# Kernel optimization log

Hardware: AMD Instinct MI355X
Metric: run time of the kernel (lower is better)

Reference implementation:

```python
import jax, jax.numpy as jnp
import numpy as np

MARGIN = 0.3  # hard-coded in all three MarginRankingLoss instances


def setup_inputs() -> dict:
    key = jax.random.key(0)
    k1, k2, k3, k4 = jax.random.split(key, 4)
    n, d, num_ids = 4096, 2048, 100
    inputs = jax.random.normal(k1, (n, d), dtype=jnp.float32)
    targets_a = jax.random.randint(k2, (n,), 0, num_ids, dtype=jnp.int64)
    targets_b = jax.random.randint(k3, (n,), 0, num_ids, dtype=jnp.int64)
    lam = jax.random.uniform(k4, (), dtype=jnp.float32)
    epoch = 60
    return {"inputs": inputs, "targets_a": targets_a, "targets_b": targets_b,
            "lam": lam, "epoch": epoch}


def reference(inputs, targets_a, targets_b, lam, epoch):
    # pairwise euclidean distance: dist[i,j] = ||x_i - x_j||
    sq = jnp.sum(inputs * inputs, axis=1)                      # [n]
    dist = sq[:, None] + sq[None, :] - 2.0 * (inputs @ inputs.T)
    dist = jnp.sqrt(jnp.clip(dist, 1e-12))                     # [n, n]

    ma = targets_a[:, None] == targets_a[None, :]
    mb = targets_b[:, None] == targets_b[None, :]
    m_same_ab = ma & mb                                        # same a AND b (incl. diagonal)
    m_same_or = (ma & ~mb) | (~ma & mb)                        # exactly one of a/b matches
    m_dif_ab = ~ma & ~mb                                       # neither matches

    ninf = -jnp.inf
    pinf = jnp.inf
    hp = jnp.max(jnp.where(m_same_ab, dist, ninf), axis=1)     # hardest positive
    hn = jnp.min(jnp.where(m_dif_ab, dist, pinf), axis=1)      # hardest negative
    max_or = jnp.max(jnp.where(m_same_or, dist, ninf), axis=1)
    min_or = jnp.min(jnp.where(m_same_or, dist, pinf), axis=1)

    use_or = m_same_or.any(axis=1) & (epoch > 50)
    sp = jnp.where(use_or, max_or, hp)
    sn = jnp.where(use_or, min_or, hn)

    # MarginRankingLoss(x1, x2, y=1) = mean(relu(x2 - x1 + margin))
    loss_1 = jnp.mean(jnp.maximum(0.0, hp - hn + MARGIN))
    loss_2 = jnp.mean(jnp.maximum(0.0, sp - hn + MARGIN))
    loss_3 = jnp.mean(jnp.maximum(0.0, hp - sn + MARGIN))
    return loss_1 + loss_2 + loss_3
```

## Files before the change

### kernel.cpp

```cpp
#include <hip/hip_runtime.h>
#include <hip/hip_bf16.h>

#define NROW 4096
#define KDIM 2048
#define ROWB (KDIM * 2)
#define BT 128
#define NB (NROW / BT)
#define BK 32
#define NT (KDIM / BK)
#define KTBUF 16384
#define AB_OFF 8192
#define PHI(r) ((((r) >> 1) & 3) << 4)

typedef __attribute__((ext_vector_type(8))) short bf16x8;
typedef __attribute__((ext_vector_type(4))) float f32x4;
typedef __attribute__((ext_vector_type(4))) unsigned short u16x4;

#define MFMA16(a, b, c) __builtin_amdgcn_mfma_f32_16x16x32_bf16((a), (b), (c), 0, 0, 0)

__device__ __forceinline__ unsigned short f2bf(float x) {
    unsigned u = __float_as_uint(x);
    unsigned r = (u + 0x7FFFu + ((u >> 16) & 1u)) >> 16;
    return (unsigned short)r;
}
__device__ __forceinline__ float bf2f(unsigned short b) {
    return __uint_as_float(((unsigned)b) << 16);
}

__global__ __launch_bounds__(256) void k_convert(const float* __restrict__ X,
                                                 unsigned short* __restrict__ Xb,
                                                 float* __restrict__ sqv,
                                                 unsigned* __restrict__ hp,
                                                 unsigned* __restrict__ hn,
                                                 unsigned* __restrict__ mor,
                                                 unsigned* __restrict__ mir,
                                                 float* __restrict__ out) {
    const int row = blockIdx.x;
    const int t = threadIdx.x;
    if (row < 16) {
        const int i = row * 256 + t;
        hp[i] = 0u;
        hn[i] = 0x7F800000u;
        mor[i] = 0u;
        mir[i] = 0x7F800000u;
        if (i == 0) out[0] = 0.f;
    }
    const float4* xr = (const float4*)(X + (size_t)row * KDIM);
    unsigned short* br = Xb + (size_t)row * KDIM;
    float acc = 0.f;
#pragma unroll
    for (int it = 0; it < 2; ++it) {
        int idx = t * 2 + it;
        float4 v = xr[idx];
        u16x4 b;
        b.x = f2bf(v.x); b.y = f2bf(v.y); b.z = f2bf(v.z); b.w = f2bf(v.w);
        float f0 = bf2f(b.x), f1 = bf2f(b.y), f2 = bf2f(b.z), f3 = bf2f(b.w);
        acc += f0 * f0 + f1 * f1 + f2 * f2 + f3 * f3;
        *(u16x4*)(br + idx * 4) = b;
    }
#pragma unroll
    for (int s = 32; s > 0; s >>= 1) acc += __shfl_xor(acc, s);
    __shared__ float red[4];
    const int lane = t & 63, wid = t >> 6;
    if (lane == 0) red[wid] = acc;
    __syncthreads();
    if (t == 0) sqv[row] = red[0] + red[1] + red[2] + red[3];
}

__global__ __launch_bounds__(256, 3) void k_gemm(const unsigned short* __restrict__ Xb,
                                                 const float* __restrict__ sqv,
                                                 const int* __restrict__ ta,
                                                 const int* __restrict__ tb,
                                                 unsigned int* __restrict__ hp,
                                                 unsigned int* __restrict__ hn,
                                                 unsigned int* __restrict__ mor,
                                                 unsigned int* __restrict__ mir) {
    __shared__ char lds[4 * KTBUF];
    int rem = blockIdx.x;
    int bi = 0;
    while (rem >= NB - bi) { rem -= NB - bi; ++bi; }
    const int bj = bi + rem;

    const int t = threadIdx.x;
    const int lane = t & 63;
    const int w = t >> 6;
    const int wm = w >> 1;
    const int wn = w & 1;
    const int l15 = lane & 15;
    const int kg16 = (lane >> 4) * 16;
    const char* xbase = (const char*)Xb;

    const int swz = ((l15 >> 1) & 3) << 4;
    const int akbase = (wm * 64 + l15) * 64 + (kg16 ^ swz);
    const int bkbase = AB_OFF + (wn * 64 + l15) * 64 + (kg16 ^ swz);

    f32x4 acc[4][4] = {};

#define STAGE(tt)                                                             \
    do {                                                                      \
        _Pragma("unroll")                                                     \
        for (int isb_ = 0; isb_ < 2; ++isb_) {                                \
            _Pragma("unroll")                                                 \
            for (int q_ = 0; q_ < 2; ++q_) {                                  \
                const int row_ = q_ * 64 + (t >> 2);                          \
                const int gr_ = (isb_ ? bj : bi) * BT + row_;                 \
                const char* gsrc_ = xbase + (size_t)gr_ * ROWB +              \
                                    (size_t)(tt) * 64 +                       \
                                    (((t & 3) * 16) ^ PHI(row_));             \
                char* ldst_ = lds + ((tt) & 3) * KTBUF + isb_ * AB_OFF +      \
                              row_ * 64 + (t & 3) * 16;                       \
                __builtin_amdgcn_global_load_lds(                             \
                    (const __attribute__((address_space(1))) void*)gsrc_,     \
                    (__attribute__((address_space(3))) void*)ldst_, 16, 0, 0);\
            }                                                                 \
        }                                                                     \
    } while (0)

    STAGE(0);
    STAGE(1);
    STAGE(2);

    for (int tk = 0; tk < NT; ++tk) {
        if (tk < NT - 2)
            asm volatile("s_waitcnt vmcnt(8)" ::: "memory");
        else if (tk == NT - 2)
            asm volatile("s_waitcnt vmcnt(4)" ::: "memory");
        else
            asm volatile("s_waitcnt vmcnt(0)" ::: "memory");
        __builtin_amdgcn_s_barrier();

        const char* buf = lds + (tk & 3) * KTBUF;
        bf16x8 af[4], bfr[4];
#pragma unroll
        for (int m = 0; m < 4; ++m)
            af[m] = *(const bf16x8*)(buf + akbase + m * 1024);
#pragma unroll
        for (int n = 0; n < 4; ++n)
            bfr[n] = *(const bf16x8*)(buf + bkbase + n * 1024);

        if (tk + 3 < NT) STAGE(tk + 3);

#pragma unroll
        for (int m = 0; m < 4; ++m)
#pragma unroll
            for (int n = 0; n < 4; ++n)
                acc[m][n] = MFMA16(af[m], bfr[n], acc[m][n]);
    }
#undef STAGE

    float sqj[4];
    int taj[4], tbj[4];
#pragma unroll
    for (int n = 0; n < 4; ++n) {
        int j = bj * BT + wn * 64 + n * 16 + l15;
        sqj[n] = sqv[j];
        taj[n] = ta[j];
        tbj[n] = tb[j];
    }
    const float INF = __uint_as_float(0x7F800000u);

    float chp[4], chn[4], cmo[4], cmi[4];
#pragma unroll
    for (int n = 0; n < 4; ++n) {
        chp[n] = 0.f; chn[n] = INF; cmo[n] = 0.f; cmi[n] = INF;
    }

#pragma unroll
    for (int m = 0; m < 4; ++m) {
#pragma unroll
        for (int reg = 0; reg < 4; ++reg) {
            const int i = bi * BT + wm * 64 + m * 16 + (lane >> 4) * 4 + reg;
            const float sqi = sqv[i];
            const int tai = ta[i], tbi = tb[i];
            float vhp = 0.f, vhn = INF, vmo = 0.f, vmi = INF;
#pragma unroll
            for (int n = 0; n < 4; ++n) {
                float d2 = fmaxf(sqi + sqj[n] - 2.f * acc[m][n][reg], 1e-12f);
                bool ma = (tai == taj[n]), mb = (tbi == tbj[n]);
                if (ma && mb) {
                    vhp = fmaxf(vhp, d2);
                    chp[n] = fmaxf(chp[n], d2);
                } else if (ma != mb) {
                    vmo = fmaxf(vmo, d2);
                    vmi = fminf(vmi, d2);
                    cmo[n] = fmaxf(cmo[n], d2);
                    cmi[n] = fminf(cmi[n], d2);
                } else {
                    vhn = fminf(vhn, d2);
                    chn[n] = fminf(chn[n], d2);
                }
            }
#pragma unroll
            for (int s = 1; s < 16; s <<= 1) {
                vhp = fmaxf(vhp, __shfl_xor(vhp, s, 16));
                vhn = fminf(vhn, __shfl_xor(vhn, s, 16));
                vmo = fmaxf(vmo, __shfl_xor(vmo, s, 16));
                vmi = fminf(vmi, __shfl_xor(vmi, s, 16));
            }
            if (l15 == 0) {
                if (vhp > 0.f) atomicMax(&hp[i], __float_as_uint(vhp));
                if (vhn < INF) atomicMin(&hn[i], __float_as_uint(vhn));
                if (vmo > 0.f) {
                    atomicMax(&mor[i], __float_as_uint(vmo));
                    atomicMin(&mir[i], __float_as_uint(vmi));
                }
            }
        }
    }

    if (bi != bj) {
#pragma unroll
        for (int n = 0; n < 4; ++n) {
            float a = chp[n], b = chn[n], c = cmo[n], d = cmi[n];
            a = fmaxf(a, __shfl_xor(a, 16)); a = fmaxf(a, __shfl_xor(a, 32));
            b = fminf(b, __shfl_xor(b, 16)); b = fminf(b, __shfl_xor(b, 32));
            c = fmaxf(c, __shfl_xor(c, 16)); c = fmaxf(c, __shfl_xor(c, 32));
            d = fminf(d, __shfl_xor(d, 16)); d = fminf(d, __shfl_xor(d, 32));
            if (lane < 16) {
                const int j = bj * BT + wn * 64 + n * 16 + lane;
                if (a > 0.f) atomicMax(&hp[j], __float_as_uint(a));
                if (b < INF) atomicMin(&hn[j], __float_as_uint(b));
                if (c > 0.f) {
                    atomicMax(&mor[j], __float_as_uint(c));
                    atomicMin(&mir[j], __float_as_uint(d));
                }
            }
        }
    }
}

__global__ __launch_bounds__(256) void k_final(const unsigned* __restrict__ hp,
                                               const unsigned* __restrict__ hn,
                                               const unsigned* __restrict__ mor,
                                               const unsigned* __restrict__ mir,
                                               const int* __restrict__ epoch_p,
                                               float* __restrict__ out) {
    const int t = threadIdx.x;
    const int i = blockIdx.x * 256 + t;
    const bool eok = (*epoch_p > 50);
    const unsigned morb = mor[i];
    float fhp = sqrtf(__uint_as_float(hp[i]));
    float fhn = sqrtf(__uint_as_float(hn[i]));
    bool use_or = (morb != 0u) && eok;
    float sp = use_or ? sqrtf(__uint_as_float(morb)) : fhp;
    float sn = use_or ? sqrtf(__uint_as_float(mir[i])) : fhn;
    float s = fmaxf(0.f, fhp - fhn + 0.3f) + fmaxf(0.f, sp - fhn + 0.3f) +
              fmaxf(0.f, fhp - sn + 0.3f);
#pragma unroll
    for (int sh = 32; sh > 0; sh >>= 1) s += __shfl_xor(s, sh);
    __shared__ float red[4];
    const int lane = t & 63, wid = t >> 6;
    if (lane == 0) red[wid] = s;
    __syncthreads();
    if (t == 0)
        atomicAdd(out, (red[0] + red[1] + red[2] + red[3]) * (1.f / 4096.f));
}

extern "C" void kernel_launch(void* const* d_in, const int* in_sizes, int n_in,
                              void* d_out, int out_size, void* d_ws, size_t ws_size,
                              hipStream_t stream) {
    const float* X = (const float*)d_in[0];
    const int* ta = (const int*)d_in[1];
    const int* tb = (const int*)d_in[2];
    const int* epoch_p = (const int*)d_in[4];
    float* out = (float*)d_out;

    char* ws = (char*)d_ws;
    unsigned short* Xb = (unsigned short*)ws;
    size_t off = (size_t)NROW * KDIM * sizeof(unsigned short);
    float* sqv = (float*)(ws + off); off += (size_t)NROW * 4;
    unsigned* hp = (unsigned*)(ws + off); off += (size_t)NROW * 4;
    unsigned* hn = (unsigned*)(ws + off); off += (size_t)NROW * 4;
    unsigned* mor = (unsigned*)(ws + off); off += (size_t)NROW * 4;
    unsigned* mir = (unsigned*)(ws + off); off += (size_t)NROW * 4;

    k_convert<<<NROW, 256, 0, stream>>>(X, Xb, sqv, hp, hn, mor, mir, out);
    k_gemm<<<(NB * (NB + 1)) / 2, 256, 0, stream>>>(Xb, sqv, ta, tb,
                                                    hp, hn, mor, mir);
    k_final<<<NROW / 256, 256, 0, stream>>>(hp, hn, mor, mir, epoch_p, out);
}
```

Measured before the change: 102.4 us.

## Double K tile to 64 and switch to two-stage LDS double buffering

Raises the K-slice per iteration from 32 to 64, which halves the number of loop iterations and barriers. The 4-deep LDS ring with three tiles in flight becomes a 2-buffer scheme with one prefetch, a full vmcnt(0) wait and an extra barrier at the end of each iteration. The XOR swizzle is widened to 8 rows to match the 128-byte row stride, and the occupancy hint drops from 3 to 2 blocks. The trade is less loop overhead against a shallower prefetch that may expose global-load latency.

```diff
diff --git a/kernel.cpp b/kernel.cpp
--- a/kernel.cpp
+++ b/kernel.cpp
@@ -6,11 +6,11 @@
 #define ROWB (KDIM * 2)
 #define BT 128
 #define NB (NROW / BT)
-#define BK 32
+#define BK 64
 #define NT (KDIM / BK)
-#define KTBUF 16384
-#define AB_OFF 8192
-#define PHI(r) ((((r) >> 1) & 3) << 4)
+#define KTBUF 32768
+#define AB_OFF 16384
+#define PHI(r) (((r) & 7) << 4)
 
 typedef __attribute__((ext_vector_type(8))) short bf16x8;
 typedef __attribute__((ext_vector_type(4))) float f32x4;
@@ -67,7 +67,7 @@
     if (t == 0) sqv[row] = red[0] + red[1] + red[2] + red[3];
 }
 
-__global__ __launch_bounds__(256, 3) void k_gemm(const unsigned short* __restrict__ Xb,
+__global__ __launch_bounds__(256, 2) void k_gemm(const unsigned short* __restrict__ Xb,
                                                  const float* __restrict__ sqv,
                                                  const int* __restrict__ ta,
                                                  const int* __restrict__ tb,
@@ -75,7 +75,7 @@
                                                  unsigned int* __restrict__ hn,
                                                  unsigned int* __restrict__ mor,
                                                  unsigned int* __restrict__ mir) {
-    __shared__ char lds[4 * KTBUF];
+    __shared__ char lds[2 * KTBUF];
     int rem = blockIdx.x;
     int bi = 0;
     while (rem >= NB - bi) { rem -= NB - bi; ++bi; }
@@ -90,9 +90,14 @@
     const int kg16 = (lane >> 4) * 16;
     const char* xbase = (const char*)Xb;
 
-    const int swz = ((l15 >> 1) & 3) << 4;
-    const int akbase = (wm * 64 + l15) * 64 + (kg16 ^ swz);
-    const int bkbase = AB_OFF + (wn * 64 + l15) * 64 + (kg16 ^ swz);
+    const int P = (l15 & 7) << 4;
+    int akb[2], bkb[2];
+#pragma unroll
+    for (int ks = 0; ks < 2; ++ks) {
+        const int kx = (ks * 64 + kg16) ^ P;
+        akb[ks] = (wm * 64 + l15) * 128 + kx;
+        bkb[ks] = AB_OFF + (wn * 64 + l15) * 128 + kx;
+    }
 
     f32x4 acc[4][4] = {};
 
@@ -101,14 +106,14 @@
         _Pragma("unroll")                                                     \
         for (int isb_ = 0; isb_ < 2; ++isb_) {                                \
             _Pragma("unroll")                                                 \
-            for (int q_ = 0; q_ < 2; ++q_) {                                  \
-                const int row_ = q_ * 64 + (t >> 2);                          \
+            for (int c_ = 0; c_ < 4; ++c_) {                                  \
+                const int row_ = c_ * 32 + (t >> 3);                          \
                 const int gr_ = (isb_ ? bj : bi) * BT + row_;                 \
                 const char* gsrc_ = xbase + (size_t)gr_ * ROWB +              \
-                                    (size_t)(tt) * 64 +                       \
-                                    (((t & 3) * 16) ^ PHI(row_));             \
-                char* ldst_ = lds + ((tt) & 3) * KTBUF + isb_ * AB_OFF +      \
-                              row_ * 64 + (t & 3) * 16;                       \
+                                    (size_t)(tt) * 128 +                      \
+                                    (((t & 7) * 16) ^ PHI(row_));             \
+                char* ldst_ = lds + ((tt) & 1) * KTBUF + isb_ * AB_OFF +      \
+                              row_ * 128 + (t & 7) * 16;                      \
                 __builtin_amdgcn_global_load_lds(                             \
                     (const __attribute__((address_space(1))) void*)gsrc_,     \
                     (__attribute__((address_space(3))) void*)ldst_, 16, 0, 0);\
@@ -117,34 +122,34 @@
     } while (0)
 
     STAGE(0);
-    STAGE(1);
-    STAGE(2);
 
     for (int tk = 0; tk < NT; ++tk) {
-        if (tk < NT - 2)
-            asm volatile("s_waitcnt vmcnt(8)" ::: "memory");
-        else if (tk == NT - 2)
-            asm volatile("s_waitcnt vmcnt(4)" ::: "memory");
-        else
-            asm volatile("s_waitcnt vmcnt(0)" ::: "memory");
+        asm volatile("s_waitcnt vmcnt(0)" ::: "memory");
         __builtin_amdgcn_s_barrier();
 
-        const char* buf = lds + (tk & 3) * KTBUF;
-        bf16x8 af[4], bfr[4];
-#pragma unroll
-        for (int m = 0; m < 4; ++m)
-            af[m] = *(const bf16x8*)(buf + akbase + m * 1024);
-#pragma unroll
-        for (int n = 0; n < 4; ++n)
-            bfr[n] = *(const bf16x8*)(buf + bkbase + n * 1024);
-
-        if (tk + 3 < NT) STAGE(tk + 3);
-
-#pragma unroll
-        for (int m = 0; m < 4; ++m)
+        const char* buf = lds + (tk & 1) * KTBUF;
+        bf16x8 af[4][2], bfr[4][2];
+#pragma unroll
+        for (int ks = 0; ks < 2; ++ks) {
+#pragma unroll
+            for (int m = 0; m < 4; ++m)
+                af[m][ks] = *(const bf16x8*)(buf + akb[ks] + m * 2048);
 #pragma unroll
             for (int n = 0; n < 4; ++n)
-                acc[m][n] = MFMA16(af[m], bfr[n], acc[m][n]);
+                bfr[n][ks] = *(const bf16x8*)(buf + bkb[ks] + n * 2048);
+        }
+
+        if (tk + 1 < NT) STAGE(tk + 1);
+
+#pragma unroll
+        for (int ks = 0; ks < 2; ++ks)
+#pragma unroll
+            for (int m = 0; m < 4; ++m)
+#pragma unroll
+                for (int n = 0; n < 4; ++n)
+                    acc[m][n] = MFMA16(af[m][ks], bfr[n][ks], acc[m][n]);
+
+        __builtin_amdgcn_s_barrier();
     }
 #undef STAGE
 
```

Measured after the change: 103.9 us. Within noise of the previous version (+1.5%).
